# Performance work log

Hardware: AMD Instinct MI355X
Metric: run time of the kernel (lower is better)

## Reference

```python
import jax, jax.numpy as jnp
import numpy as np

SHIFT = 1  # module's random shift_direction, fixed to +1 for determinism
B, C, H, W_SP = 1024, 512, 7, 7


def setup_inputs() -> dict:
    key = jax.random.key(0)
    k1, k2 = jax.random.split(key)
    x = jax.random.normal(k1, (B, C, H, W_SP), dtype=jnp.float32)
    W = jax.random.normal(k2, (256, 3, 3, 512), dtype=jnp.float32)
    return {"x": x, "W": W}


def _forward(x, W):
    # unfold along H with kernel (3,1), padding (1,0):
    # patches[b,c,kh,h,w] = x_padded[b,c,h+kh,w]
    xp = jnp.pad(x, ((0, 0), (0, 0), (1, 1), (0, 0)))
    t2 = jnp.stack([xp[:, :, k:k + H, :] for k in range(3)], axis=2)  # (B,512,3,7,7)
    # split channels 512 -> (2,256), move group dim next to H
    t2 = t2.reshape(B, 2, 256, 3, H, W_SP)
    t2 = t2.transpose(0, 2, 3, 4, 1, 5)          # (B,256,3,7,2,7)
    t2 = t2.reshape(B, 256, 3, 14, W_SP)         # interleave (h,group) -> 14
    t2 = jnp.roll(t2, SHIFT, axis=3)             # shift along interleaved dim
    t2 = t2.reshape(B, 256, 3, 7, 2, W_SP).sum(axis=4)  # (B,256,3,7,7)
    t2 = t2.transpose(0, 1, 3, 2, 4)             # (B,256,7,3,7) = (m,l,n,j,w)
    # second shift + unfold along w with kernel 3, padding 1
    t3 = jnp.roll(t2, SHIFT, axis=4)
    tp = jnp.pad(t3, ((0, 0), (0, 0), (0, 0), (0, 0), (1, 1)))
    t3u = jnp.stack([tp[..., k:k + W_SP] for k in range(3)], axis=4)  # (B,256,7,3,3,7) = (m,l,n,j,k,p)
    # torch einsum 'mlnjok, ljki -> mnoi' with o = output position, k = kernel tap
    out = jnp.einsum('mlnjkp,ljki->mpni', t3u, W)  # wait: check axis order below
    # Note: torch permutes (m,c,h,j,kernel,pos)->(m,c,h,j,pos,kernel) before einsum,
    # so contraction is over (l,j,kernel) and output is (m, n=h, o=pos, i).
    out = jnp.einsum('mlnjkp,ljki->mnpi', t3u, W)  # (B,7,7,512)
    return out.transpose(0, 3, 1, 2)              # (B,512,7,7)


def reference(x, W):
    return _forward(x, W)
```

## Files before the change

### kernel.cpp

```cpp
#include <hip/hip_runtime.h>
#include <hip/hip_bf16.h>


typedef __bf16 bf16x8 __attribute__((ext_vector_type(8)));
typedef float f32x4 __attribute__((ext_vector_type(4)));

__global__ __launch_bounds__(256) void prep_w(const float* __restrict__ Wg,
                                              __bf16* __restrict__ W2) {
    int idx = blockIdx.x * 256 + threadIdx.x;
    int i = idx / 2304;
    int kk = idx - i * 2304;
    int tap = kk / 768;
    int c = kk - tap * 768;
    W2[idx] = (__bf16)Wg[(c * 3 + tap) * 512 + i];
}

__global__ __launch_bounds__(256) void gemm_shift(const float* __restrict__ x,
                                                  const __bf16* __restrict__ W2,
                                                  float* __restrict__ out) {
    __shared__ __bf16 T[16 * 10 * 40];
    __shared__ __bf16 Bt[128 * 104];

    const int tid = threadIdx.x;
    const int mb = blockIdx.x >> 2;
    const int nb = blockIdx.x & 3;
    const int i0 = nb * 128;

    const int cl  = tid & 31;
    const int bh0 = tid >> 5;
    const int bhg0 = mb * 16 + bh0;
    const int bhg1 = bhg0 + 8;
    const int b0 = bhg0 / 7, h0 = bhg0 - 7 * b0;
    const int b1 = bhg1 / 7, h1 = bhg1 - 7 * b1;
    const int hm0 = (h0 + 6) % 7, hm1 = (h1 + 6) % 7;

    for (int q = tid; q < 16 * 10 * 40 / 2; q += 256) ((int*)T)[q] = 0;

    const int lane = tid & 63;
    const int wave = tid >> 6;
    const int wm = wave >> 1;
    const int wn = wave & 1;
    const int ln15 = lane & 15;
    const int g = lane >> 4;

    f32x4 acc[4][4];
    #pragma unroll
    for (int a = 0; a < 4; ++a)
        #pragma unroll
        for (int b = 0; b < 4; ++b) acc[a][b] = (f32x4){0.f, 0.f, 0.f, 0.f};

    for (int chunk = 0; chunk < 24; ++chunk) {
        const int cg = chunk * 32 + cl;
        const int l = cg / 3;
        const int j = cg - 3 * l;
        {
            const int r1 = h0 + j - 1, r2 = hm0 + j - 1;
            float v[7] = {0.f, 0.f, 0.f, 0.f, 0.f, 0.f, 0.f};
            if (r1 >= 0 && r1 < 7) {
                const float* p1 = x + (((size_t)b0 * 512 + l) * 7 + r1) * 7;
                #pragma unroll
                for (int w = 0; w < 7; ++w) v[w] += p1[w];
            }
            if (r2 >= 0 && r2 < 7) {
                const float* p2 = x + (((size_t)b0 * 512 + 256 + l) * 7 + r2) * 7;
                #pragma unroll
                for (int w = 0; w < 7; ++w) v[w] += p2[w];
            }
            #pragma unroll
            for (int w = 0; w < 7; ++w)
                T[bh0 * 400 + ((w + 1) % 7 + 1) * 40 + cl] = (__bf16)v[w];
        }
        {
            const int r1 = h1 + j - 1, r2 = hm1 + j - 1;
            float v[7] = {0.f, 0.f, 0.f, 0.f, 0.f, 0.f, 0.f};
            if (r1 >= 0 && r1 < 7) {
                const float* p1 = x + (((size_t)b1 * 512 + l) * 7 + r1) * 7;
                #pragma unroll
                for (int w = 0; w < 7; ++w) v[w] += p1[w];
            }
            if (r2 >= 0 && r2 < 7) {
                const float* p2 = x + (((size_t)b1 * 512 + 256 + l) * 7 + r2) * 7;
                #pragma unroll
                for (int w = 0; w < 7; ++w) v[w] += p2[w];
            }
            #pragma unroll
            for (int w = 0; w < 7; ++w)
                T[(bh0 + 8) * 400 + ((w + 1) % 7 + 1) * 40 + cl] = (__bf16)v[w];
        }

        #pragma unroll
        for (int it = 0; it < 6; ++it) {
            const int u = it * 256 + tid;
            const int tap = u >> 9;
            const int rem = u & 511;
            const int n = rem >> 2;
            const int q = rem & 3;
            const float4 val = *(const float4*)(W2 + (size_t)(i0 + n) * 2304 +
                                                tap * 768 + chunk * 32 + q * 8);
            *(float4*)(&Bt[n * 104 + tap * 32 + q * 8]) = val;
        }

        __syncthreads();

        #pragma unroll
        for (int tap = 0; tap < 3; ++tap) {
            bf16x8 af[4], bfr[4];
            #pragma unroll
            for (int mf = 0; mf < 4; ++mf) {
                const int bh_l = wm * 8 + mf * 2 + (ln15 >> 3);
                const int p = ln15 & 7;
                af[mf] = *(const bf16x8*)(&T[(bh_l * 10 + p + tap) * 40 + g * 8]);
            }
            #pragma unroll
            for (int nf = 0; nf < 4; ++nf) {
                const int n_l = wn * 64 + nf * 16 + ln15;
                bfr[nf] = *(const bf16x8*)(&Bt[n_l * 104 + tap * 32 + g * 8]);
            }
            #pragma unroll
            for (int mf = 0; mf < 4; ++mf)
                #pragma unroll
                for (int nf = 0; nf < 4; ++nf)
                    acc[mf][nf] = __builtin_amdgcn_mfma_f32_16x16x32_bf16(
                        af[mf], bfr[nf], acc[mf][nf], 0, 0, 0);
        }

        __syncthreads();
    }

    #pragma unroll
    for (int mf = 0; mf < 4; ++mf) {
        #pragma unroll
        for (int r = 0; r < 4; ++r) {
            const int mrow = g * 4 + r;
            const int Mg_l = wm * 64 + mf * 16 + mrow;
            const int p = Mg_l & 7;
            if (p == 7) continue;
            const int bh_l = Mg_l >> 3;
            const int bhg = mb * 16 + bh_l;
            const int b = bhg / 7;
            const int h = bhg - 7 * b;
            #pragma unroll
            for (int nf = 0; nf < 4; ++nf) {
                const int i = i0 + wn * 64 + nf * 16 + ln15;
                out[(((size_t)b * 512 + i) * 7 + h) * 7 + p] = acc[mf][nf][r];
            }
        }
    }
}

extern "C" void kernel_launch(void* const* d_in, const int* in_sizes, int n_in,
                              void* d_out, int out_size, void* d_ws, size_t ws_size,
                              hipStream_t stream) {
    const float* x  = (const float*)d_in[0];
    const float* Wg = (const float*)d_in[1];
    float* out = (float*)d_out;
    __bf16* W2 = (__bf16*)d_ws;

    prep_w<<<dim3(512 * 2304 / 256), dim3(256), 0, stream>>>(Wg, W2);
    gemm_shift<<<dim3(448 * 4), dim3(256), 0, stream>>>(x, W2, out);
}
```

Measured before the change: 440.8 us.

## Precompute shifted bf16 activation tensor and stream it into GEMM tiles

Adds a prep_v kernel that builds the shifted, summed and unfolded activations once as a bf16 matrix in workspace, laid out so that 16-byte vector loads can fill the GEMM's A tile. The new gemm_vt kernel reads these rows instead of recomputing the shift and sum from fp32 x with scalar loads in every N block, and it remaps block indices so that the four N blocks sharing an M tile run close together. This removes the fourfold redundant gather from x. The cost is an extra kernel launch and about 77 MB of extra global write and read traffic, and the old path stays as a fallback when the workspace is too small.

```diff
diff --git a/kernel.cpp b/kernel.cpp
--- a/kernel.cpp
+++ b/kernel.cpp
@@ -4,6 +4,10 @@
 
 typedef __bf16 bf16x8 __attribute__((ext_vector_type(8)));
 typedef float f32x4 __attribute__((ext_vector_type(4)));
+
+#define VT_OFFSET (4u << 20)
+#define VT_BYTES  (7168ull * 7 * 768 * 2)
+#define WS_NEED   (VT_OFFSET + VT_BYTES)
 
 __global__ __launch_bounds__(256) void prep_w(const float* __restrict__ Wg,
                                               __bf16* __restrict__ W2) {
@@ -15,6 +19,140 @@
     W2[idx] = (__bf16)Wg[(c * 3 + tap) * 512 + i];
 }
 
+__global__ __launch_bounds__(256) void prep_v(const float* __restrict__ x,
+                                              __bf16* __restrict__ Vt) {
+    const int b = blockIdx.x;
+    const int l = threadIdx.x;
+    float xa[49], xb[49];
+    const float* pa = x + ((size_t)b * 512 + l) * 49;
+    const float* pb = x + ((size_t)b * 512 + 256 + l) * 49;
+    #pragma unroll
+    for (int q = 0; q < 49; ++q) xa[q] = pa[q];
+    #pragma unroll
+    for (int q = 0; q < 49; ++q) xb[q] = pb[q];
+
+    #pragma unroll
+    for (int h = 0; h < 7; ++h) {
+        const int hm = (h + 6) % 7;
+        #pragma unroll
+        for (int j = 0; j < 3; ++j) {
+            const int r1 = h + j - 1;
+            const int r2 = hm + j - 1;
+            __bf16* dst = Vt + (size_t)(b * 7 + h) * 7 * 768 + (l * 3 + j);
+            #pragma unroll
+            for (int w = 0; w < 7; ++w) {
+                float v = 0.f;
+                if (r1 >= 0 && r1 < 7) v += xa[r1 * 7 + w];
+                if (r2 >= 0 && r2 < 7) v += xb[r2 * 7 + w];
+                dst[(size_t)((w + 1) % 7) * 768] = (__bf16)v;
+            }
+        }
+    }
+}
+
+__global__ __launch_bounds__(256) void gemm_vt(const __bf16* __restrict__ Vt,
+                                               const __bf16* __restrict__ W2,
+                                               float* __restrict__ out) {
+    __shared__ __bf16 T[16 * 400];
+    __shared__ __bf16 Bt[128 * 104];
+
+    const int tid = threadIdx.x;
+    const int g0 = blockIdx.x;
+    const int nb = (g0 >> 3) & 3;
+    const int mb = ((g0 >> 5) << 3) | (g0 & 7);
+    const int i0 = nb * 128;
+
+    for (int q = tid; q < 3200; q += 256) ((int*)T)[q] = 0;
+
+    const int lane = tid & 63;
+    const int wave = tid >> 6;
+    const int wm = wave >> 1;
+    const int wn = wave & 1;
+    const int ln15 = lane & 15;
+    const int gq = lane >> 4;
+
+    f32x4 acc[4][4];
+    #pragma unroll
+    for (int a = 0; a < 4; ++a)
+        #pragma unroll
+        for (int bq = 0; bq < 4; ++bq) acc[a][bq] = (f32x4){0.f, 0.f, 0.f, 0.f};
+
+    __syncthreads();
+
+    for (int chunk = 0; chunk < 24; ++chunk) {
+        #pragma unroll
+        for (int it = 0; it < 2; ++it) {
+            const int u = it * 256 + tid;
+            if (u < 448) {
+                const int q = u & 3;
+                const int tmp = u >> 2;
+                const int t = tmp % 7;
+                const int bh = tmp / 7;
+                const float4 val = *(const float4*)(
+                    Vt + (size_t)((mb * 16 + bh) * 7 + t) * 768 + chunk * 32 + q * 8);
+                *(float4*)(&T[bh * 400 + (t + 1) * 40 + q * 8]) = val;
+            }
+        }
+        #pragma unroll
+        for (int it = 0; it < 6; ++it) {
+            const int u = it * 256 + tid;
+            const int tap = u >> 9;
+            const int rem = u & 511;
+            const int n = rem >> 2;
+            const int q = rem & 3;
+            const float4 val = *(const float4*)(W2 + (size_t)(i0 + n) * 2304 +
+                                                tap * 768 + chunk * 32 + q * 8);
+            *(float4*)(&Bt[n * 104 + tap * 32 + q * 8]) = val;
+        }
+
+        __syncthreads();
+
+        #pragma unroll
+        for (int tap = 0; tap < 3; ++tap) {
+            bf16x8 af[4], bfr[4];
+            #pragma unroll
+            for (int mf = 0; mf < 4; ++mf) {
+                const int bh_l = wm * 8 + mf * 2 + (ln15 >> 3);
+                const int p = ln15 & 7;
+                af[mf] = *(const bf16x8*)(&T[(bh_l * 10 + p + tap) * 40 + gq * 8]);
+            }
+            #pragma unroll
+            for (int nf = 0; nf < 4; ++nf) {
+                const int n_l = wn * 64 + nf * 16 + ln15;
+                bfr[nf] = *(const bf16x8*)(&Bt[n_l * 104 + tap * 32 + gq * 8]);
+            }
+            #pragma unroll
+            for (int mf = 0; mf < 4; ++mf)
+                #pragma unroll
+                for (int nf = 0; nf < 4; ++nf)
+                    acc[mf][nf] = __builtin_amdgcn_mfma_f32_16x16x32_bf16(
+                        af[mf], bfr[nf], acc[mf][nf], 0, 0, 0);
+        }
+
+        __syncthreads();
+    }
+
+    #pragma unroll
+    for (int mf = 0; mf < 4; ++mf) {
+        #pragma unroll
+        for (int r = 0; r < 4; ++r) {
+            const int mrow = gq * 4 + r;
+            const int Mg_l = wm * 64 + mf * 16 + mrow;
+            const int p = Mg_l & 7;
+            if (p == 7) continue;
+            const int bh_l = Mg_l >> 3;
+            const int bhg = mb * 16 + bh_l;
+            const int b = bhg / 7;
+            const int h = bhg - 7 * b;
+            #pragma unroll
+            for (int nf = 0; nf < 4; ++nf) {
+                const int i = i0 + wn * 64 + nf * 16 + ln15;
+                out[(((size_t)b * 512 + i) * 7 + h) * 7 + p] = acc[mf][nf][r];
+            }
+        }
+    }
+}
+
 __global__ __launch_bounds__(256) void gemm_shift(const float* __restrict__ x,
                                                   const __bf16* __restrict__ W2,
                                                   float* __restrict__ out) {
@@ -41,13 +179,15 @@
     const int wm = wave >> 1;
     const int wn = wave & 1;
     const int ln15 = lane & 15;
-    const int g = lane >> 4;
+    const int gq = lane >> 4;
 
     f32x4 acc[4][4];
     #pragma unroll
     for (int a = 0; a < 4; ++a)
         #pragma unroll
-        for (int b = 0; b < 4; ++b) acc[a][b] = (f32x4){0.f, 0.f, 0.f, 0.f};
+        for (int bq = 0; bq < 4; ++bq) acc[a][bq] = (f32x4){0.f, 0.f, 0.f, 0.f};
+
+    __syncthreads();
 
     for (int chunk = 0; chunk < 24; ++chunk) {
         const int cg = chunk * 32 + cl;
@@ -109,12 +249,12 @@
             for (int mf = 0; mf < 4; ++mf) {
                 const int bh_l = wm * 8 + mf * 2 + (ln15 >> 3);
                 const int p = ln15 & 7;
-                af[mf] = *(const bf16x8*)(&T[(bh_l * 10 + p + tap) * 40 + g * 8]);
+                af[mf] = *(const bf16x8*)(&T[(bh_l * 10 + p + tap) * 40 + gq * 8]);
             }
             #pragma unroll
             for (int nf = 0; nf < 4; ++nf) {
                 const int n_l = wn * 64 + nf * 16 + ln15;
-                bfr[nf] = *(const bf16x8*)(&Bt[n_l * 104 + tap * 32 + g * 8]);
+                bfr[nf] = *(const bf16x8*)(&Bt[n_l * 104 + tap * 32 + gq * 8]);
             }
             #pragma unroll
             for (int mf = 0; mf < 4; ++mf)
@@ -131,7 +271,7 @@
     for (int mf = 0; mf < 4; ++mf) {
         #pragma unroll
         for (int r = 0; r < 4; ++r) {
-            const int mrow = g * 4 + r;
+            const int mrow = gq * 4 + r;
             const int Mg_l = wm * 64 + mf * 16 + mrow;
             const int p = Mg_l & 7;
             if (p == 7) continue;
@@ -157,5 +297,12 @@
     __bf16* W2 = (__bf16*)d_ws;
 
     prep_w<<<dim3(512 * 2304 / 256), dim3(256), 0, stream>>>(Wg, W2);
-    gemm_shift<<<dim3(448 * 4), dim3(256), 0, stream>>>(x, W2, out);
-}
+
+    if (ws_size >= WS_NEED) {
+        __bf16* Vt = (__bf16*)((char*)d_ws + VT_OFFSET);
+        prep_v<<<dim3(1024), dim3(256), 0, stream>>>(x, Vt);
+        gemm_vt<<<dim3(448 * 4), dim3(256), 0, stream>>>(Vt, W2, out);
+    } else {
+        gemm_shift<<<dim3(448 * 4), dim3(256), 0, stream>>>(x, W2, out);
+    }
+}
```

Result: faster. 381.9 us (-13.4%).

## Precompute shifted bf16 activation tensor in a prep kernel, then run GEMM from it

Applied to the files above, without the earlier changes.

Adds a prep kernel that builds the shifted, summed, bf16 activation matrix (bh, w, channel*tap) in workspace, staging x rows through shared memory for coalesced reads. The GEMM kernel then loads A tiles with vectorized 16-byte copies instead of recomputing the shifts with scattered scalar fp32 loads. The GEMM block drops to 128 threads, each wave now covers all 128 N columns with a 4x8 accumulator tile, and blocks are remapped for locality. This adds an extra global write and read of the intermediate tensor plus more register pressure per thread.

```diff
diff --git a/kernel.cpp b/kernel.cpp
--- a/kernel.cpp
+++ b/kernel.cpp
@@ -4,6 +4,10 @@
 
 typedef __bf16 bf16x8 __attribute__((ext_vector_type(8)));
 typedef float f32x4 __attribute__((ext_vector_type(4)));
+
+#define VT_OFFSET (4u << 20)
+#define VT_BYTES  (7168ull * 7 * 768 * 2)
+#define WS_NEED   (VT_OFFSET + VT_BYTES)
 
 __global__ __launch_bounds__(256) void prep_w(const float* __restrict__ Wg,
                                               __bf16* __restrict__ W2) {
@@ -15,82 +19,110 @@
     W2[idx] = (__bf16)Wg[(c * 3 + tap) * 512 + i];
 }
 
-__global__ __launch_bounds__(256) void gemm_shift(const float* __restrict__ x,
-                                                  const __bf16* __restrict__ W2,
-                                                  float* __restrict__ out) {
-    __shared__ __bf16 T[16 * 10 * 40];
+__global__ __launch_bounds__(256) void prep_v2(const float* __restrict__ x,
+                                               __bf16* __restrict__ Vt) {
+    __shared__ float XA[3][256][8];
+    __shared__ float XB[3][256][8];
+    const int tid = threadIdx.x;
+    const int bh = blockIdx.x;
+    const int b = bh / 7, h = bh - 7 * b;
+    const int hm = (h + 6) % 7;
+
+    #pragma unroll
+    for (int jr = 0; jr < 3; ++jr) {
+        const int ra = h + jr - 1;
+        if (ra >= 0 && ra < 7) {
+            const float* src = x + (((size_t)b * 512) * 7 + ra) * 7;
+            #pragma unroll
+            for (int it = 0; it < 7; ++it) {
+                const int idx = it * 256 + tid;
+                const int l = idx / 7, w = idx - 7 * l;
+                XA[jr][l][w] = src[l * 49 + w];
+            }
+        } else {
+            #pragma unroll
+            for (int it = 0; it < 8; ++it)
+                ((float*)XA[jr])[it * 256 + tid] = 0.f;
+        }
+        const int rb = hm + jr - 1;
+        if (rb >= 0 && rb < 7) {
+            const float* src = x + (((size_t)b * 512 + 256) * 7 + rb) * 7;
+            #pragma unroll
+            for (int it = 0; it < 7; ++it) {
+                const int idx = it * 256 + tid;
+                const int l = idx / 7, w = idx - 7 * l;
+                XB[jr][l][w] = src[l * 49 + w];
+            }
+        } else {
+            #pragma unroll
+            for (int it = 0; it < 8; ++it)
+                ((float*)XB[jr])[it * 256 + tid] = 0.f;
+        }
+    }
+    __syncthreads();
+
+    #pragma unroll
+    for (int it = 0; it < 3; ++it) {
+        const int u = it * 256 + tid;
+        if (u < 672) {
+            const int r = u / 96, cu = u - 96 * r;
+            const int w = (r + 6) % 7;
+            bf16x8 v;
+            #pragma unroll
+            for (int e = 0; e < 8; ++e) {
+                const int c = cu * 8 + e;
+                const int l = c / 3, j = c - 3 * l;
+                v[e] = (__bf16)(XA[j][l][w] + XB[j][l][w]);
+            }
+            *(bf16x8*)(Vt + (size_t)bh * 5376 + u * 8) = v;
+        }
+    }
+}
+
+__global__ __launch_bounds__(128, 2) void gemm_vt2(const __bf16* __restrict__ Vt,
+                                                   const __bf16* __restrict__ W2,
+                                                   float* __restrict__ out) {
+    __shared__ __bf16 T[16 * 400];
     __shared__ __bf16 Bt[128 * 104];
 
     const int tid = threadIdx.x;
-    const int mb = blockIdx.x >> 2;
-    const int nb = blockIdx.x & 3;
+    const int g0 = blockIdx.x;
+    const int nb = (g0 >> 3) & 3;
+    const int mb = ((g0 >> 5) << 3) | (g0 & 7);
     const int i0 = nb * 128;
 
-    const int cl  = tid & 31;
-    const int bh0 = tid >> 5;
-    const int bhg0 = mb * 16 + bh0;
-    const int bhg1 = bhg0 + 8;
-    const int b0 = bhg0 / 7, h0 = bhg0 - 7 * b0;
-    const int b1 = bhg1 / 7, h1 = bhg1 - 7 * b1;
-    const int hm0 = (h0 + 6) % 7, hm1 = (h1 + 6) % 7;
-
-    for (int q = tid; q < 16 * 10 * 40 / 2; q += 256) ((int*)T)[q] = 0;
+    for (int q = tid; q < 3200; q += 128) ((int*)T)[q] = 0;
 
     const int lane = tid & 63;
     const int wave = tid >> 6;
-    const int wm = wave >> 1;
-    const int wn = wave & 1;
     const int ln15 = lane & 15;
-    const int g = lane >> 4;
+    const int gq = lane >> 4;
 
-    f32x4 acc[4][4];
+    f32x4 acc[4][8];
     #pragma unroll
     for (int a = 0; a < 4; ++a)
         #pragma unroll
-        for (int b = 0; b < 4; ++b) acc[a][b] = (f32x4){0.f, 0.f, 0.f, 0.f};
+        for (int bq = 0; bq < 8; ++bq) acc[a][bq] = (f32x4){0.f, 0.f, 0.f, 0.f};
+
+    __syncthreads();
 
     for (int chunk = 0; chunk < 24; ++chunk) {
-        const int cg = chunk * 32 + cl;
-        const int l = cg / 3;
-        const int j = cg - 3 * l;
-        {
-            const int r1 = h0 + j - 1, r2 = hm0 + j - 1;
-            float v[7] = {0.f, 0.f, 0.f, 0.f, 0.f, 0.f, 0.f};
-            if (r1 >= 0 && r1 < 7) {
-                const float* p1 = x + (((size_t)b0 * 512 + l) * 7 + r1) * 7;
-                #pragma unroll
-                for (int w = 0; w < 7; ++w) v[w] += p1[w];
+        #pragma unroll
+        for (int it = 0; it < 4; ++it) {
+            const int u = it * 128 + tid;
+            if (u < 448) {
+                const int q = u & 3;
+                const int tmp = u >> 2;
+                const int t = tmp % 7;
+                const int bh = tmp / 7;
+                const float4 val = *(const float4*)(
+                    Vt + (size_t)((mb * 16 + bh) * 7 + t) * 768 + chunk * 32 + q * 8);
+                *(float4*)(&T[bh * 400 + (t + 1) * 40 + q * 8]) = val;
             }
-            if (r2 >= 0 && r2 < 7) {
-                const float* p2 = x + (((size_t)b0 * 512 + 256 + l) * 7 + r2) * 7;
-                #pragma unroll
-                for (int w = 0; w < 7; ++w) v[w] += p2[w];
-            }
-            #pragma unroll
-            for (int w = 0; w < 7; ++w)
-                T[bh0 * 400 + ((w + 1) % 7 + 1) * 40 + cl] = (__bf16)v[w];
         }
-        {
-            const int r1 = h1 + j - 1, r2 = hm1 + j - 1;
-            float v[7] = {0.f, 0.f, 0.f, 0.f, 0.f, 0.f, 0.f};
-            if (r1 >= 0 && r1 < 7) {
-                const float* p1 = x + (((size_t)b1 * 512 + l) * 7 + r1) * 7;
-                #pragma unroll
-                for (int w = 0; w < 7; ++w) v[w] += p1[w];
-            }
-            if (r2 >= 0 && r2 < 7) {
-                const float* p2 = x + (((size_t)b1 * 512 + 256 + l) * 7 + r2) * 7;
-                #pragma unroll
-                for (int w = 0; w < 7; ++w) v[w] += p2[w];
-            }
-            #pragma unroll
-            for (int w = 0; w < 7; ++w)
-                T[(bh0 + 8) * 400 + ((w + 1) % 7 + 1) * 40 + cl] = (__bf16)v[w];
-        }
-
         #pragma unroll
-        for (int it = 0; it < 6; ++it) {
-            const int u = it * 256 + tid;
+        for (int it = 0; it < 12; ++it) {
+            const int u = it * 128 + tid;
             const int tap = u >> 9;
             const int rem = u & 511;
             const int n = rem >> 2;
@@ -104,22 +136,22 @@
 
         #pragma unroll
         for (int tap = 0; tap < 3; ++tap) {
-            bf16x8 af[4], bfr[4];
+            bf16x8 af[4], bfr[8];
             #pragma unroll
             for (int mf = 0; mf < 4; ++mf) {
-                const int bh_l = wm * 8 + mf * 2 + (ln15 >> 3);
+                const int bh_l = wave * 8 + mf * 2 + (ln15 >> 3);
                 const int p = ln15 & 7;
-                af[mf] = *(const bf16x8*)(&T[(bh_l * 10 + p + tap) * 40 + g * 8]);
+                af[mf] = *(const bf16x8*)(&T[(bh_l * 10 + p + tap) * 40 + gq * 8]);
             }
             #pragma unroll
-            for (int nf = 0; nf < 4; ++nf) {
-                const int n_l = wn * 64 + nf * 16 + ln15;
-                bfr[nf] = *(const bf16x8*)(&Bt[n_l * 104 + tap * 32 + g * 8]);
+            for (int nf = 0; nf < 8; ++nf) {
+                const int n_l = nf * 16 + ln15;
+                bfr[nf] = *(const bf16x8*)(&Bt[n_l * 104 + tap * 32 + gq * 8]);
             }
             #pragma unroll
             for (int mf = 0; mf < 4; ++mf)
                 #pragma unroll
-                for (int nf = 0; nf < 4; ++nf)
+                for (int nf = 0; nf < 8; ++nf)
                     acc[mf][nf] = __builtin_amdgcn_mfma_f32_16x16x32_bf16(
                         af[mf], bfr[nf], acc[mf][nf], 0, 0, 0);
         }
@@ -131,8 +163,8 @@
     for (int mf = 0; mf < 4; ++mf) {
         #pragma unroll
         for (int r = 0; r < 4; ++r) {
-            const int mrow = g * 4 + r;
-            const int Mg_l = wm * 64 + mf * 16 + mrow;
+            const int mrow = gq * 4 + r;
+            const int Mg_l = wave * 64 + mf * 16 + mrow;
             const int p = Mg_l & 7;
             if (p == 7) continue;
             const int bh_l = Mg_l >> 3;
@@ -140,8 +172,8 @@
             const int b = bhg / 7;
             const int h = bhg - 7 * b;
             #pragma unroll
-            for (int nf = 0; nf < 4; ++nf) {
-                const int i = i0 + wn * 64 + nf * 16 + ln15;
+            for (int nf = 0; nf < 8; ++nf) {
+                const int i = i0 + nf * 16 + ln15;
                 out[(((size_t)b * 512 + i) * 7 + h) * 7 + p] = acc[mf][nf][r];
             }
         }
@@ -155,7 +187,9 @@
     const float* Wg = (const float*)d_in[1];
     float* out = (float*)d_out;
     __bf16* W2 = (__bf16*)d_ws;
+    __bf16* Vt = (__bf16*)((char*)d_ws + VT_OFFSET);
 
     prep_w<<<dim3(512 * 2304 / 256), dim3(256), 0, stream>>>(Wg, W2);
-    gemm_shift<<<dim3(448 * 4), dim3(256), 0, stream>>>(x, W2, out);
+    prep_v2<<<dim3(7168), dim3(256), 0, stream>>>(x, Vt);
+    gemm_vt2<<<dim3(448 * 4), dim3(128), 0, stream>>>(Vt, W2, out);
 }
```

Result: slower. 499.2 us (+13.2%).
